# Performance work log

Hardware: AMD Instinct MI355X
Metric: run time of the kernel (lower is better)

Reference implementation:

```python
import jax, jax.numpy as jnp
import numpy as np

B, T, C, V = 4, 2048, 1024, 50257


def setup_inputs() -> dict:
    key = jax.random.key(0)
    k1, k2, k3 = jax.random.split(key, 3)
    x = jax.random.normal(k1, (B, T, C), dtype=jnp.float32)
    y = jax.random.randint(k2, (B, T), 0, V, dtype=jnp.int64)
    # nn.Linear(C, V): weight [V, C], bias [V]
    W = jax.random.normal(k3, (V, C), dtype=jnp.float32) * (1.0 / np.sqrt(C))
    b = jnp.zeros((V,), dtype=jnp.float32)
    return {"x": x, "y": y, "W": W, "b": b}


def reference(x, y, W, b):
    # logits: [B*T, V]
    logits = jnp.einsum("btc,vc->btv", x, W).reshape(B * T, V) + b
    labels = y.reshape(-1)  # [B*T]
    logp = jax.nn.log_softmax(logits, axis=-1)
    nll = -jnp.take_along_axis(logp, labels[:, None], axis=-1)[:, 0]
    return jnp.mean(nll)
```

## Files before the change

### kernel.cpp

```cpp
#include <hip/hip_runtime.h>


#define M_TOT 8192
#define K_TOT 1024
#define V_TOT 50257
#define NVB   197
#define NPAD  (NVB * 256)
#define PSTRIDE (NVB * 2)
#define KB    (K_TOT / 64)
#define GSTRIDE ((long)KB * 64 * 32)

typedef __attribute__((ext_vector_type(8)))  int   int8v;
typedef __attribute__((ext_vector_type(16))) float floatx16;

__device__ __forceinline__ int f4_to_fp8x4(float4 v) {
  int r = __builtin_amdgcn_cvt_pk_fp8_f32(v.x, v.y, 0, false);
  r = __builtin_amdgcn_cvt_pk_fp8_f32(v.z, v.w, r, true);
  return r;
}

__global__ __launch_bounds__(256) void pack_kernel(
    const float* __restrict__ src, char* __restrict__ dst, int nrows) {
  const int kb = blockIdx.x, g = blockIdx.y;
  const int i = threadIdx.x;
  const int r = i >> 3, seg = i & 7;
  const int srow = g * 32 + r;
  int lo = 0, hi = 0;
  if (srow < nrows) {
    const float4* s = (const float4*)(src + (long)srow * K_TOT + kb * 64 + seg * 8);
    lo = f4_to_fp8x4(s[0]);
    hi = f4_to_fp8x4(s[1]);
  }
  const int h = seg >> 2;
  const int q = (seg >> 1) & 1;
  char* d = dst + ((long)(g * KB + kb) * 2048 +
                   (q * 64 + h * 32 + r) * 16 + (seg & 1) * 8);
  *(int2*)d = make_int2(lo, hi);
}

#define GLOAD16(gp, lp)                                              \
  __builtin_amdgcn_global_load_lds(                                  \
      (const __attribute__((address_space(1))) void*)(gp),           \
      (__attribute__((address_space(3))) void*)(lp), 16, 0, 0)

__device__ __forceinline__ int8v read_frag(const char* p) {
  int4 lo = *(const int4*)p;
  int4 hi = *(const int4*)(p + 1024);
  int8v r;
  r[0] = lo.x; r[1] = lo.y; r[2] = lo.z; r[3] = lo.w;
  r[4] = hi.x; r[5] = hi.y; r[6] = hi.z; r[7] = hi.w;
  return r;
}

__global__ __launch_bounds__(512, 2) void gemm_lse_kernel(
    const char* __restrict__ pW, const char* __restrict__ pX,
    const float* __restrict__ bias, float* __restrict__ psum) {
  __shared__ char sm[3][32768];

  const int tid  = threadIdx.x;
  const int wid  = tid >> 6;
  const int lane = tid & 63;
  const int wv   = wid >> 2;
  const int wb   = wid & 3;
  const int mblk = blockIdx.x;
  const int vblk = blockIdx.y;

  const char* srcA = pW + (long)(vblk * 8 + wid) * GSTRIDE + lane * 16;
  const char* srcB = pX + (long)(mblk * 8 + wid) * GSTRIDE + lane * 16;

  auto stage = [&](int o) {
    char* dA = &sm[0][0] + o + wid * 2048;
    char* dB = &sm[0][0] + o + 16384 + wid * 2048;
    GLOAD16(srcA,        dA);
    GLOAD16(srcA + 1024, dA + 1024);
    GLOAD16(srcB,        dB);
    GLOAD16(srcB + 1024, dB + 1024);
    srcA += 2048;
    srcB += 2048;
  };

  const int rdAoff = (wv * 4) * 2048 + lane * 16;
  const int rdBoff = 16384 + (wb * 2) * 2048 + lane * 16;

  floatx16 acc[4][2] = {};

  stage(0);
  stage(32768);

  int curo = 0;
  int stgo = 65536;
#pragma unroll 1
  for (int t = 0; t < 16; ++t) {
    asm volatile("s_waitcnt vmcnt(4)" ::: "memory");
    __builtin_amdgcn_s_barrier();
    asm volatile("" ::: "memory");
    const char* ba = &sm[0][0] + curo;
    int8v a[4], b[2];
#pragma unroll
    for (int tn = 0; tn < 2; ++tn) b[tn] = read_frag(ba + rdBoff + tn * 2048);
#pragma unroll
    for (int tv = 0; tv < 4; ++tv) a[tv] = read_frag(ba + rdAoff + tv * 2048);
    stage(stgo);
    __builtin_amdgcn_s_setprio(1);
#pragma unroll
    for (int tv = 0; tv < 4; ++tv)
#pragma unroll
      for (int tn = 0; tn < 2; ++tn)
        acc[tv][tn] = __builtin_amdgcn_mfma_scale_f32_32x32x64_f8f6f4(
            a[tv], b[tn], acc[tv][tn], 0, 0, 0, 0x7F7F7F7F, 0, 0x7F7F7F7F);
    __builtin_amdgcn_s_setprio(0);
    curo = (curo == 65536) ? 0 : curo + 32768;
    stgo = (stgo == 65536) ? 0 : stgo + 32768;
  }

  const int half = lane >> 5, l32 = lane & 31;
  const int vbase = vblk * 256 + wv * 128 + 4 * half;
  float s0 = 0.0f, s1 = 0.0f;
#pragma unroll
  for (int tv = 0; tv < 4; ++tv) {
#pragma unroll
    for (int reg = 0; reg < 16; ++reg) {
      int v = vbase + tv * 32 + (reg & 3) + 8 * (reg >> 2);
      float bv = (v < V_TOT) ? bias[v] : -1e30f;
      s0 += __expf(acc[tv][0][reg] + bv);
      s1 += __expf(acc[tv][1][reg] + bv);
    }
  }
  s0 += __shfl_xor(s0, 32, 64);
  s1 += __shfl_xor(s1, 32, 64);
  if (half == 0) {
    int m = mblk * 256 + wb * 64 + l32;
    long base = (long)m * PSTRIDE + vblk * 2 + wv;
    psum[base] = s0;
    psum[base + (long)32 * PSTRIDE] = s1;
  }
}

__global__ __launch_bounds__(256) void finalize_kernel(
    const float* __restrict__ psum, const float* __restrict__ x,
    const float* __restrict__ W, const float* __restrict__ b,
    const int* __restrict__ y, float* __restrict__ loss) {
  const int wave = threadIdx.x >> 6;
  const int lane = threadIdx.x & 63;
  const int r = blockIdx.x * 4 + wave;

  const float* ps = psum + (long)r * PSTRIDE;
  float s = 0.0f;
  for (int j = lane; j < PSTRIDE; j += 64) s += ps[j];
#pragma unroll
  for (int o = 1; o < 64; o <<= 1) s += __shfl_xor(s, o, 64);

  int label = y[r];
  const float4* xr = (const float4*)(x + (long)r * K_TOT);
  const float4* wr = (const float4*)(W + (long)label * K_TOT);
  float d = 0.0f;
  for (int j = lane; j < K_TOT / 4; j += 64) {
    float4 a = xr[j], w = wr[j];
    d += a.x * w.x + a.y * w.y + a.z * w.z + a.w * w.w;
  }
#pragma unroll
  for (int o = 1; o < 64; o <<= 1) d += __shfl_xor(d, o, 64);

  if (lane == 0) loss[r] = logf(s) - d - b[label];
}

__global__ __launch_bounds__(256) void reduce_kernel(
    const float* __restrict__ loss, float* __restrict__ out) {
  const int tid = threadIdx.x;
  float s = 0.0f;
  for (int j = tid; j < M_TOT; j += 256) s += loss[j];
#pragma unroll
  for (int o = 1; o < 64; o <<= 1) s += __shfl_xor(s, o, 64);
  __shared__ float wsum[4];
  if ((tid & 63) == 0) wsum[tid >> 6] = s;
  __syncthreads();
  if (tid == 0)
    out[0] = (wsum[0] + wsum[1] + wsum[2] + wsum[3]) * (1.0f / (float)M_TOT);
}

extern "C" void kernel_launch(void* const* d_in, const int* in_sizes, int n_in,
                              void* d_out, int out_size, void* d_ws, size_t ws_size,
                              hipStream_t stream) {
  (void)in_sizes; (void)n_in; (void)out_size; (void)ws_size;
  const float* x = (const float*)d_in[0];
  const int*   y = (const int*)d_in[1];
  const float* W = (const float*)d_in[2];
  const float* b = (const float*)d_in[3];
  float* out = (float*)d_out;

  char* ws = (char*)d_ws;
  const size_t PX_BYTES = (size_t)M_TOT * K_TOT;
  const size_t PW_BYTES = (size_t)NPAD * K_TOT;
  const size_t PS_BYTES = (size_t)M_TOT * PSTRIDE * 4;
  char*  pX   = ws;
  char*  pW   = ws + PX_BYTES;
  float* psum = (float*)(ws + PX_BYTES + PW_BYTES);
  float* loss = (float*)(ws + PX_BYTES + PW_BYTES + PS_BYTES);

  pack_kernel<<<dim3(KB, M_TOT / 32), 256, 0, stream>>>(x, pX, M_TOT);
  pack_kernel<<<dim3(KB, NPAD / 32), 256, 0, stream>>>(W, pW, V_TOT);
  gemm_lse_kernel<<<dim3(M_TOT / 256, NVB), 512, 0, stream>>>(pW, pX, b, psum);
  finalize_kernel<<<M_TOT / 4, 256, 0, stream>>>(psum, x, W, b, y, loss);
  reduce_kernel<<<1, 256, 0, stream>>>(loss, out);
}
```

Baseline: 740.1 us.

## Deepen LDS ring to four stages and prefetch next A fragments into registers

```diff
diff --git a/kernel.cpp b/kernel.cpp
--- a/kernel.cpp
+++ b/kernel.cpp
@@ -52,10 +52,35 @@
   return r;
 }
 
+#define KSTEP(AC, AN)                                                        \
+  asm volatile("s_waitcnt vmcnt(4)" ::: "memory");                           \
+  __builtin_amdgcn_s_barrier();                                              \
+  asm volatile("" ::: "memory");                                             \
+  _Pragma("unroll")                                                          \
+  for (int tn = 0; tn < 2; ++tn)                                             \
+    bb[tn] = read_frag(&sm[0][0] + bo_cur + rdBoff + tn * 2048);             \
+  __builtin_amdgcn_sched_barrier(0);  \
+  _Pragma("unroll")                                                          \
+  for (int tv = 0; tv < 4; ++tv)                                             \
+    AN[tv] = read_frag(&sm[0][0] + bo_nxt + rdAoff + tv * 2048);             \
+  stage(bo_stg);                                                             \
+  __builtin_amdgcn_sched_barrier(0);      \
+  __builtin_amdgcn_s_setprio(1);                                             \
+  _Pragma("unroll")                                                          \
+  for (int tv = 0; tv < 4; ++tv)                                             \
+    _Pragma("unroll")                                                        \
+    for (int tn = 0; tn < 2; ++tn)                                           \
+      acc[tv][tn] = __builtin_amdgcn_mfma_scale_f32_32x32x64_f8f6f4(         \
+          AC[tv], bb[tn], acc[tv][tn], 0, 0, 0, 0x7F7F7F7F, 0, 0x7F7F7F7F);  \
+  __builtin_amdgcn_s_setprio(0);                                             \
+  bo_cur = (bo_cur + 32768) & 131071;                                        \
+  bo_nxt = (bo_nxt + 32768) & 131071;                                        \
+  bo_stg = (bo_stg + 32768) & 131071;
+
 __global__ __launch_bounds__(512, 2) void gemm_lse_kernel(
     const char* __restrict__ pW, const char* __restrict__ pX,
     const float* __restrict__ bias, float* __restrict__ psum) {
-  __shared__ char sm[3][32768];
+  __shared__ char sm[4][32768];
 
   const int tid  = threadIdx.x;
   const int wid  = tid >> 6;
@@ -68,50 +93,38 @@
   const char* srcA = pW + (long)(vblk * 8 + wid) * GSTRIDE + lane * 16;
   const char* srcB = pX + (long)(mblk * 8 + wid) * GSTRIDE + lane * 16;
 
+  const int dstAoff = wid * 2048;
+  const int dstBoff = 16384 + wid * 2048;
+  const int rdAoff  = (wv * 4) * 2048 + lane * 16;
+  const int rdBoff  = 16384 + (wb * 2) * 2048 + lane * 16;
+
   auto stage = [&](int o) {
-    char* dA = &sm[0][0] + o + wid * 2048;
-    char* dB = &sm[0][0] + o + 16384 + wid * 2048;
-    GLOAD16(srcA,        dA);
-    GLOAD16(srcA + 1024, dA + 1024);
-    GLOAD16(srcB,        dB);
-    GLOAD16(srcB + 1024, dB + 1024);
+    GLOAD16(srcA,        &sm[0][0] + o + dstAoff);
+    GLOAD16(srcA + 1024, &sm[0][0] + o + dstAoff + 1024);
+    GLOAD16(srcB,        &sm[0][0] + o + dstBoff);
+    GLOAD16(srcB + 1024, &sm[0][0] + o + dstBoff + 1024);
     srcA += 2048;
     srcB += 2048;
   };
 
-  const int rdAoff = (wv * 4) * 2048 + lane * 16;
-  const int rdBoff = 16384 + (wb * 2) * 2048 + lane * 16;
-
   floatx16 acc[4][2] = {};
-
-  stage(0);
-  stage(32768);
-
-  int curo = 0;
-  int stgo = 65536;
+  int8v aE[4], aO[4], bb[2];
+
+  stage(0); stage(32768); stage(65536);
+  asm volatile("s_waitcnt vmcnt(8)" ::: "memory");
+  __builtin_amdgcn_s_barrier();
+  asm volatile("" ::: "memory");
+#pragma unroll
+  for (int tv = 0; tv < 4; ++tv)
+    aE[tv] = read_frag(&sm[0][0] + rdAoff + tv * 2048);
+
+  int bo_cur = 0, bo_nxt = 32768, bo_stg = 98304;
 #pragma unroll 1
-  for (int t = 0; t < 16; ++t) {
-    asm volatile("s_waitcnt vmcnt(4)" ::: "memory");
-    __builtin_amdgcn_s_barrier();
-    asm volatile("" ::: "memory");
-    const char* ba = &sm[0][0] + curo;
-    int8v a[4], b[2];
-#pragma unroll
-    for (int tn = 0; tn < 2; ++tn) b[tn] = read_frag(ba + rdBoff + tn * 2048);
-#pragma unroll
-    for (int tv = 0; tv < 4; ++tv) a[tv] = read_frag(ba + rdAoff + tv * 2048);
-    stage(stgo);
-    __builtin_amdgcn_s_setprio(1);
-#pragma unroll
-    for (int tv = 0; tv < 4; ++tv)
-#pragma unroll
-      for (int tn = 0; tn < 2; ++tn)
-        acc[tv][tn] = __builtin_amdgcn_mfma_scale_f32_32x32x64_f8f6f4(
-            a[tv], b[tn], acc[tv][tn], 0, 0, 0, 0x7F7F7F7F, 0, 0x7F7F7F7F);
-    __builtin_amdgcn_s_setprio(0);
-    curo = (curo == 65536) ? 0 : curo + 32768;
-    stgo = (stgo == 65536) ? 0 : stgo + 32768;
-  }
+  for (int it = 0; it < 8; ++it) {
+    KSTEP(aE, aO)
+    KSTEP(aO, aE)
+  }
+  asm volatile("s_waitcnt vmcnt(0)" ::: "memory");
 
   const int half = lane >> 5, l32 = lane & 31;
   const int vbase = vblk * 256 + wv * 128 + 4 * half;
```

After: 749.3 us. Within noise of the previous version (+1.2%).
